# Kernel tuning notes

Measured on AMD Instinct MI355X. Metric: run time of the kernel, lower is better.

## Reference

```python
import jax, jax.numpy as jnp
import numpy as np

D = 1024   # dim_model
H = 16     # num_heads
DH = D // H  # per-head dim for k and v
B, S = 2, 2048
EPS = 1e-5


def layer_norm(x, g, b):
    mu = jnp.mean(x, axis=-1, keepdims=True)
    var = jnp.var(x, axis=-1, keepdims=True)
    return (x - mu) * jax.lax.rsqrt(var + EPS) * g + b


def setup_inputs() -> dict:
    key = jax.random.key(0)
    ks = jax.random.split(key, 8)
    s_d = 1.0 / np.sqrt(D)
    inp = {
        "x": jax.random.normal(ks[0], (B, S, D), dtype=jnp.float32),
        # stacked per-head projections, [H, D, DH] (torch Linear weight.T per head)
        "wq": jax.random.uniform(ks[1], (H, D, DH), jnp.float32, -s_d, s_d),
        "wk": jax.random.uniform(ks[2], (H, D, DH), jnp.float32, -s_d, s_d),
        "wv": jax.random.uniform(ks[3], (H, D, DH), jnp.float32, -s_d, s_d),
        "wo": jax.random.uniform(ks[4], (D, D), jnp.float32, -s_d, s_d),
        "w1": jax.random.uniform(ks[5], (D, D), jnp.float32, -s_d, s_d),  # FFN hidden == dim_model per source
        "w2": jax.random.uniform(ks[6], (D, D), jnp.float32, -s_d, s_d),
        "ln1_g": jnp.ones((D,), jnp.float32), "ln1_b": jnp.zeros((D,), jnp.float32),
        "ln2_g": jnp.ones((D,), jnp.float32), "ln2_b": jnp.zeros((D,), jnp.float32),
        "ln3_g": jnp.ones((D,), jnp.float32), "ln3_b": jnp.zeros((D,), jnp.float32),
    }
    return inp


def reference(x, wq, wk, wv, wo, w1, w2, ln1_g, ln1_b, ln2_g, ln2_b, ln3_g, ln3_b):
    residual = x
    h = layer_norm(x, ln1_g, ln1_b)  # pre_attention_norm
    # batched multi-head attention (equivalent to per-head loop + concat)
    q = jnp.einsum("bsd,hdk->bhsk", h, wq)
    k = jnp.einsum("bsd,hdk->bhsk", h, wk)
    v = jnp.einsum("bsd,hdk->bhsk", h, wv)
    scores = jnp.einsum("bhsk,bhtk->bhst", q, k) / jnp.sqrt(jnp.float32(DH))
    attn = jax.nn.softmax(scores, axis=-1)
    ctx = jnp.einsum("bhst,bhtk->bhsk", attn, v)        # [B,H,S,DH]
    concat = ctx.transpose(0, 2, 1, 3).reshape(x.shape[0], x.shape[1], -1)  # head concat order
    h = concat @ wo
    h = h + residual
    h = layer_norm(h, ln2_g, ln2_b)  # post_attention_norm (dropout is identity, rate=0)
    residual = h
    ffn = jnp.maximum(h @ w1, 0.0) @ w2
    h = ffn + residual
    h = layer_norm(h, ln3_g, ln3_b)  # post_ffn_norm
    return h
```

## Files before the change

### kernel.cpp

```cpp
#include <hip/hip_runtime.h>
#include <stdint.h>

typedef unsigned short u16;
typedef __attribute__((ext_vector_type(8))) short short8;
typedef __attribute__((ext_vector_type(4))) short short4v;
typedef __attribute__((ext_vector_type(4))) float f32x4;

#define DEV static __device__ __forceinline__

constexpr int DMODEL = 1024;
constexpr int SEQ = 2048;

DEV u16 f2b(float f){
  uint32_t u = __float_as_uint(f);
  u += 0x7FFF + ((u >> 16) & 1);
  return (u16)(u >> 16);
}

#define AS1(p) ((const __attribute__((address_space(1))) void*)(p))
#define AS3(p) ((__attribute__((address_space(3))) void*)(p))
#define GLOAD_LDS16(g, l) __builtin_amdgcn_global_load_lds(AS1(g), AS3(l), 16, 0, 0)
#define LDSADDR(p) ((uint32_t)(size_t)((__attribute__((address_space(3))) void*)(p)))

DEV short4v ds_tr16(uint32_t a){
  short4v r;
  asm volatile("ds_read_b64_tr_b16 %0, %1" : "=v"(r) : "v"(a) : "memory");
  return r;
}

DEV void pswap(uint32_t &a, uint32_t &b){
  asm("v_permlane32_swap_b32 %0, %1":"+v"(a),"+v"(b));
  asm("v_permlane16_swap_b32 %0, %1":"+v"(a),"+v"(b));
}

DEV uint32_t cvtpk(float lo, float hi){
  uint32_t r; asm("v_cvt_pk_bf16_f32 %0, %1, %2":"=v"(r):"v"(lo),"v"(hi)); return r;
}

__global__ __launch_bounds__(256) void transpose_generic(
    const float* __restrict__ src, u16* __restrict__ dst, int R, int C){
  __shared__ float tile[64][65];
  int r0 = blockIdx.x*64, c0 = blockIdx.y*64;
  int j = threadIdx.x & 63, i0 = threadIdx.x >> 6;
  for(int i=i0;i<64;i+=4) tile[i][j] = src[(size_t)(r0+i)*C + c0 + j];
  __syncthreads();
  int ii = threadIdx.x & 63, jj0 = threadIdx.x >> 6;
  for(int jj=jj0;jj<64;jj+=4) dst[(size_t)(c0+jj)*R + r0 + ii] = f2b(tile[ii][jj]);
}

__global__ __launch_bounds__(256) void transpose_qkv(
    const float* __restrict__ wq, const float* __restrict__ wk,
    const float* __restrict__ wv, u16* __restrict__ dst){
  int z = blockIdx.z, p = z>>4, h = z&15;
  const float* src = (p==0?wq:(p==1?wk:wv)) + (size_t)h*1024*64;
  float sc = (p==0) ? 0.18033688011112042f : 1.0f;
  __shared__ float tile[64][65];
  int r0 = blockIdx.x*64;
  int j = threadIdx.x & 63, i0 = threadIdx.x >> 6;
  for(int i=i0;i<64;i+=4) tile[i][j] = src[(size_t)(r0+i)*64 + j];
  __syncthreads();
  u16* drow = dst + ((size_t)p*1024 + h*64)*1024;
  int ii = threadIdx.x & 63, jj0 = threadIdx.x >> 6;
  for(int jj=jj0;jj<64;jj+=4) drow[(size_t)jj*1024 + r0 + ii] = f2b(tile[ii][jj]*sc);
}

__global__ __launch_bounds__(256) void ln_kernel(
    const float* __restrict__ in, const float* __restrict__ g, const float* __restrict__ bb,
    u16* __restrict__ outb, float* __restrict__ outf){
  int row = blockIdx.x, tid = threadIdx.x;
  const float4* x4 = (const float4*)(in + (size_t)row*DMODEL);
  float4 v = x4[tid];
  float s  = v.x+v.y+v.z+v.w;
  float ss = v.x*v.x + v.y*v.y + v.z*v.z + v.w*v.w;
  #pragma unroll
  for(int m=1;m<64;m<<=1){ s += __shfl_xor(s,m); ss += __shfl_xor(ss,m); }
  __shared__ float red[8];
  int w = tid>>6;
  if((tid&63)==0){ red[w]=s; red[4+w]=ss; }
  __syncthreads();
  s  = red[0]+red[1]+red[2]+red[3];
  ss = red[4]+red[5]+red[6]+red[7];
  float mu  = s*(1.f/DMODEL);
  float var = ss*(1.f/DMODEL) - mu*mu;
  float rs  = rsqrtf(var + 1e-5f);
  float4 gv = ((const float4*)g)[tid];
  float4 bv = ((const float4*)bb)[tid];
  float y0=(v.x-mu)*rs*gv.x+bv.x, y1=(v.y-mu)*rs*gv.y+bv.y;
  float y2=(v.z-mu)*rs*gv.z+bv.z, y3=(v.w-mu)*rs*gv.w+bv.w;
  if(outb){ ushort4 o = make_ushort4(f2b(y0),f2b(y1),f2b(y2),f2b(y3));
            ((ushort4*)outb)[(size_t)row*(DMODEL/4) + tid] = o; }
  if(outf){ ((float4*)outf)[(size_t)row*(DMODEL/4) + tid] = make_float4(y0,y1,y2,y3); }
}

template<int MODE>
__global__ __launch_bounds__(256) void gemm_bt(
    const u16* __restrict__ A, const u16* __restrict__ BT, int M, int N, int K,
    float* __restrict__ outf, u16* __restrict__ outb, const float* __restrict__ res,
    u16* __restrict__ oq, u16* __restrict__ ok, u16* __restrict__ ov){
  __shared__ u16 lsA[4][2048];
  __shared__ u16 lsB[4][4096];
  int n0 = blockIdx.x*128, m0 = blockIdx.y*64;
  int tid = threadIdx.x, lane = tid&63, w = tid>>6;
  int wr = w>>1, wc = w&1, rq = lane&15, hk = lane>>4;
  int oa = tid*16;
  int ob0 = tid*16, ob1 = 4096 + tid*16;
  const u16* aS  = A  + (size_t)(m0 + (oa>>6))*K  + ((oa&63)>>1);
  const u16* bS0 = BT + (size_t)(n0 + (ob0>>6))*K + ((ob0&63)>>1);
  const u16* bS1 = BT + (size_t)(n0 + (ob1>>6))*K + ((ob1&63)>>1);
  int nk = K>>5;
  f32x4 acc[2][4] = {};
  #pragma unroll
  for(int t=0;t<3;++t){
    GLOAD_LDS16(aS  + t*32, &lsA[t][w*512]);
    GLOAD_LDS16(bS0 + t*32, &lsB[t][w*512]);
    GLOAD_LDS16(bS1 + t*32, &lsB[t][2048 + w*512]);
  }
  for(int kt=0; kt<nk; ++kt){
    if(kt < nk-2)       asm volatile("s_waitcnt vmcnt(6)" ::: "memory");
    else if(kt == nk-2) asm volatile("s_waitcnt vmcnt(3)" ::: "memory");
    else                asm volatile("s_waitcnt vmcnt(0)" ::: "memory");
    __builtin_amdgcn_s_barrier();
    __builtin_amdgcn_sched_barrier(0);
    if(kt+3 < nk){
      int nb = (kt+3)&3;
      GLOAD_LDS16(aS  + (kt+3)*32, &lsA[nb][w*512]);
      GLOAD_LDS16(bS0 + (kt+3)*32, &lsB[nb][w*512]);
      GLOAD_LDS16(bS1 + (kt+3)*32, &lsB[nb][2048 + w*512]);
    }
    const u16* la = &lsA[kt&3][0];
    const u16* lb = &lsB[kt&3][0];
    short8 aF[2], bF[4];
    #pragma unroll
    for(int m=0;m<2;++m) aF[m] = *(const short8*)(la + (wr*32 + m*16 + rq)*32 + hk*8);
    #pragma unroll
    for(int n=0;n<4;++n) bF[n] = *(const short8*)(lb + (wc*64 + n*16 + rq)*32 + hk*8);
    __builtin_amdgcn_s_setprio(1);
    #pragma unroll
    for(int m=0;m<2;++m){
      #pragma unroll
      for(int n=0;n<4;++n)
        acc[m][n] = __builtin_amdgcn_mfma_f32_16x16x32_bf16(aF[m], bF[n], acc[m][n], 0,0,0);
    }
    __builtin_amdgcn_s_setprio(0);
  }
  #pragma unroll
  for(int m=0;m<2;++m){
    #pragma unroll
    for(int n=0;n<4;++n){
      int rb = m0 + wr*32 + m*16 + (hk<<2);
      int c  = n0 + wc*64 + n*16 + rq;
      #pragma unroll
      for(int qq=0;qq<4;++qq){
        int r = rb+qq; float val = acc[m][n][qq];
        if constexpr(MODE==1){
          int proj=c>>10, n1=c&1023, h=n1>>6, d2=n1&63;
          int b=r>>11, si=r&2047;
          u16* dst = proj==0?oq:(proj==1?ok:ov);
          dst[(((size_t)(b*16+h))*SEQ + si)*64 + d2] = f2b(val);
        } else if constexpr(MODE==2){
          outf[(size_t)r*N + c] = val + res[(size_t)r*N + c];
        } else if constexpr(MODE==3){
          outb[(size_t)r*N + c] = f2b(val>0.f?val:0.f);
        } else {
          outb[(size_t)r*N + c] = f2b(val);
        }
      }
    }
  }
}

__global__ __launch_bounds__(256) void attn_kernel(
    const u16* __restrict__ q, const u16* __restrict__ k, const u16* __restrict__ v,
    u16* __restrict__ concat){
  __shared__ u16 lsK[2][4096];
  __shared__ u16 lsV[2][4096];
  int qt = blockIdx.x, bh = blockIdx.y;
  const u16* qp = q + (size_t)bh*SEQ*64;
  const u16* kp = k + (size_t)bh*SEQ*64;
  const u16* vp = v + (size_t)bh*SEQ*64;
  int tid=threadIdx.x, lane=tid&63, w=tid>>6;
  int rq = lane&15, hk = lane>>4;
  const uint32_t sw = (uint32_t)((rq&7)<<4);

  short8 aQ[2];
  {
    const u16* qrow = qp + (size_t)(qt*64 + w*16 + rq)*64 + hk*8;
    aQ[0] = *(const short8*)(qrow);
    aQ[1] = *(const short8*)(qrow + 32);
  }
  short8 bOnes;
  #pragma unroll
  for(int j=0;j<8;++j) bOnes[j] = (short)0x3F80;

  int o0 = tid*16,        kr0 = o0>>7;
  int o1 = 4096 + tid*16, kr1 = o1>>7;
  int koff0 = kr0*64 + ((((o0&127) ^ ((kr0&7)<<4)))>>1);
  int koff1 = kr1*64 + ((((o1&127) ^ ((kr1&7)<<4)))>>1);
  auto vdec = [](int c)->int{
    int t  = ((c>>5)<<2) | ((c&7)>>1);
    int d8 = (((c>>3)&3)<<1) | (c&1);
    return t*64 + d8*8;
  };
  int voff0 = vdec(tid), voff1 = vdec(256+tid);

  f32x4 accO[4] = {};
  f32x4 accL = {};

  GLOAD_LDS16(kp + koff0, &lsK[0][0   + w*512]);
  GLOAD_LDS16(kp + koff1, &lsK[0][2048+ w*512]);
  GLOAD_LDS16(vp + voff0, &lsV[0][0   + w*512]);
  GLOAD_LDS16(vp + voff1, &lsV[0][2048+ w*512]);

  int cur = 0;
  for(int kt=0; kt<SEQ/64; ++kt){
    __syncthreads();
    if(kt+1 < SEQ/64){
      int b = cur^1;
      const u16* ksrc = kp + (kt+1)*4096;
      const u16* vsrc = vp + (kt+1)*4096;
      GLOAD_LDS16(ksrc + koff0, &lsK[b][0   + w*512]);
      GLOAD_LDS16(ksrc + koff1, &lsK[b][2048+ w*512]);
      GLOAD_LDS16(vsrc + voff0, &lsV[b][0   + w*512]);
      GLOAD_LDS16(vsrc + voff1, &lsV[b][2048+ w*512]);
    }
    const char* kb = (const char*)&lsK[cur][0];
    short8 bK[4][2];
    #pragma unroll
    for(int ts=0;ts<4;++ts){
      uint32_t rb = (uint32_t)((ts*16+rq)*128);
      bK[ts][0] = *(const short8*)(kb + rb + (((0u<<6)|(uint32_t)(hk<<4)) ^ sw));
      bK[ts][1] = *(const short8*)(kb + rb + (((1u<<6)|(uint32_t)(hk<<4)) ^ sw));
    }
    f32x4 z[4];
    __builtin_amdgcn_s_setprio(1);
    #pragma unroll
    for(int ts=0;ts<4;++ts){
      f32x4 zz = {};
      zz = __builtin_amdgcn_mfma_f32_16x16x32_bf16(bK[ts][0], aQ[0], zz, 0,0,0);
      zz = __builtin_amdgcn_mfma_f32_16x16x32_bf16(bK[ts][1], aQ[1], zz, 0,0,0);
      z[ts] = zz;
    }
    __builtin_amdgcn_s_setprio(0);
    uint32_t vA = LDSADDR(&lsV[cur][0]) + (uint32_t)(hk*1024 + rq*2);
    short4v vL[2][4][2];
    #pragma unroll
    for(int kh=0;kh<2;++kh){
      #pragma unroll
      for(int ds=0;ds<4;++ds){
        vL[kh][ds][0] = ds_tr16(vA + kh*4096 + ds*128);
        vL[kh][ds][1] = ds_tr16(vA + kh*4096 + ds*128 + 512);
      }
    }
    #pragma unroll
    for(int ts=0;ts<4;++ts){
      #pragma unroll
      for(int r=0;r<4;++r)
        z[ts][r] = __builtin_exp2f(z[ts][r]);
    }
    uint32_t u00=cvtpk(z[0][0],z[0][1]), u01=cvtpk(z[0][2],z[0][3]);
    uint32_t u10=cvtpk(z[1][0],z[1][1]), u11=cvtpk(z[1][2],z[1][3]);
    uint32_t u20=cvtpk(z[2][0],z[2][1]), u21=cvtpk(z[2][2],z[2][3]);
    uint32_t u30=cvtpk(z[3][0],z[3][1]), u31=cvtpk(z[3][2],z[3][3]);
    pswap(u00,u10); pswap(u01,u11);
    pswap(u20,u30); pswap(u21,u31);
    union U8 { uint32_t d[4]; short8 v; } ap0, ap1;
    ap0.d[0]=u00; ap0.d[1]=u01; ap0.d[2]=u10; ap0.d[3]=u11;
    ap1.d[0]=u20; ap1.d[1]=u21; ap1.d[2]=u30; ap1.d[3]=u31;
    asm volatile("s_waitcnt lgkmcnt(0)" ::: "memory");
    __builtin_amdgcn_sched_barrier(0);
    __builtin_amdgcn_s_setprio(1);
    #pragma unroll
    for(int kh=0;kh<2;++kh){
      short8 aP = kh ? ap1.v : ap0.v;
      accL = __builtin_amdgcn_mfma_f32_16x16x32_bf16(aP, bOnes, accL, 0,0,0);
      #pragma unroll
      for(int ds=0;ds<4;++ds){
        short8 bV = __builtin_shufflevector(vL[kh][ds][0], vL[kh][ds][1], 0,1,2,3,4,5,6,7);
        accO[ds] = __builtin_amdgcn_mfma_f32_16x16x32_bf16(aP, bV, accO[ds], 0,0,0);
      }
    }
    __builtin_amdgcn_s_setprio(0);
    cur ^= 1;
  }
  int b = bh>>4, h = bh&15;
  #pragma unroll
  for(int r=0;r<4;++r){
    float inv = 1.f / accL[r];
    int si = qt*64 + w*16 + hk*4 + r;
    #pragma unroll
    for(int ds=0;ds<4;++ds){
      int c = h*64 + ds*16 + rq;
      concat[((size_t)b*SEQ + si)*DMODEL + c] = f2b(accO[ds][r] * inv);
    }
  }
}

extern "C" void kernel_launch(void* const* d_in, const int* in_sizes, int n_in,
                              void* d_out, int out_size, void* d_ws, size_t ws_size,
                              hipStream_t stream){
  (void)in_sizes; (void)n_in; (void)out_size; (void)ws_size;
  const float* x    = (const float*)d_in[0];
  const float* wq   = (const float*)d_in[1];
  const float* wk   = (const float*)d_in[2];
  const float* wv   = (const float*)d_in[3];
  const float* wo   = (const float*)d_in[4];
  const float* w1   = (const float*)d_in[5];
  const float* w2   = (const float*)d_in[6];
  const float* ln1g = (const float*)d_in[7];
  const float* ln1b = (const float*)d_in[8];
  const float* ln2g = (const float*)d_in[9];
  const float* ln2b = (const float*)d_in[10];
  const float* ln3g = (const float*)d_in[11];
  const float* ln3b = (const float*)d_in[12];
  float* out = (float*)d_out;

  char* ws = (char*)d_ws; size_t off = 0;
  auto alloc = [&](size_t b)->char*{ char* p = ws + off; off += (b + 255) & ~(size_t)255; return p; };
  u16*   WqkvT = (u16*)  alloc((size_t)3072*1024*2);
  u16*   WoT   = (u16*)  alloc((size_t)1024*1024*2);
  u16*   W1T   = (u16*)  alloc((size_t)1024*1024*2);
  u16*   W2T   = (u16*)  alloc((size_t)1024*1024*2);
  u16*   h1    = (u16*)  alloc((size_t)4096*1024*2);
  u16*   qb    = (u16*)  alloc((size_t)4194304*2);
  u16*   kb    = (u16*)  alloc((size_t)4194304*2);
  u16*   vb    = (u16*)  alloc((size_t)4194304*2);
  u16*   cc    = (u16*)  alloc((size_t)4096*1024*2);
  float* r1    = (float*)alloc((size_t)4096*1024*4);
  u16*   h2b   = (u16*)  alloc((size_t)4096*1024*2);
  float* h2f   = (float*)alloc((size_t)4096*1024*4);
  u16*   ffn1  = h1;
  float* r2    = r1;

  transpose_qkv<<<dim3(16,1,48),256,0,stream>>>(wq,wk,wv,WqkvT);
  transpose_generic<<<dim3(16,16),256,0,stream>>>(wo,WoT,1024,1024);
  transpose_generic<<<dim3(16,16),256,0,stream>>>(w1,W1T,1024,1024);
  transpose_generic<<<dim3(16,16),256,0,stream>>>(w2,W2T,1024,1024);

  ln_kernel<<<4096,256,0,stream>>>(x, ln1g, ln1b, h1, nullptr);
  gemm_bt<1><<<dim3(24,64),256,0,stream>>>(h1,WqkvT,4096,3072,1024,
      nullptr,nullptr,nullptr, qb,kb,vb);
  attn_kernel<<<dim3(32,32),256,0,stream>>>(qb,kb,vb,cc);
  gemm_bt<2><<<dim3(8,64),256,0,stream>>>(cc,WoT,4096,1024,1024,
      r1,nullptr,x, nullptr,nullptr,nullptr);
  ln_kernel<<<4096,256,0,stream>>>(r1, ln2g, ln2b, h2b, h2f);
  gemm_bt<3><<<dim3(8,64),256,0,stream>>>(h2b,W1T,4096,1024,1024,
      nullptr,ffn1,nullptr, nullptr,nullptr,nullptr);
  gemm_bt<2><<<dim3(8,64),256,0,stream>>>(ffn1,W2T,4096,1024,1024,
      r2,nullptr,h2f, nullptr,nullptr,nullptr);
  ln_kernel<<<4096,256,0,stream>>>(r2, ln3g, ln3b, nullptr, out);
}
```

Measured before the change: 221.1 us.

## Enlarge GEMM and attention tiles, store QKV interleaved, merge weight transposes

GEMM block tile grows from 64x128 to 128x128, doubling per-block A loads and accumulators. The attention kernel now processes 128 query rows per block, two 16-row groups per wave, so each K/V tile loaded into LDS is reused twice as much. The QKV projection writes a plain row-major [4096,3072] buffer that attention reads with strided addressing, removing the scatter epilogue. The four weight-transpose launches are merged into one. Larger tiles raise register pressure and cut the block count, which may hurt occupancy and load balance.

```diff
diff --git a/kernel.cpp b/kernel.cpp
--- a/kernel.cpp
+++ b/kernel.cpp
@@ -37,31 +37,35 @@
   uint32_t r; asm("v_cvt_pk_bf16_f32 %0, %1, %2":"=v"(r):"v"(lo),"v"(hi)); return r;
 }
 
-__global__ __launch_bounds__(256) void transpose_generic(
-    const float* __restrict__ src, u16* __restrict__ dst, int R, int C){
+__global__ __launch_bounds__(256) void transpose_all(
+    const float* __restrict__ wq, const float* __restrict__ wk,
+    const float* __restrict__ wv, const float* __restrict__ wo,
+    const float* __restrict__ w1, const float* __restrict__ w2,
+    u16* __restrict__ WqkvT, u16* __restrict__ WoT,
+    u16* __restrict__ W1T, u16* __restrict__ W2T){
   __shared__ float tile[64][65];
-  int r0 = blockIdx.x*64, c0 = blockIdx.y*64;
+  int bid = blockIdx.x;
   int j = threadIdx.x & 63, i0 = threadIdx.x >> 6;
-  for(int i=i0;i<64;i+=4) tile[i][j] = src[(size_t)(r0+i)*C + c0 + j];
-  __syncthreads();
-  int ii = threadIdx.x & 63, jj0 = threadIdx.x >> 6;
-  for(int jj=jj0;jj<64;jj+=4) dst[(size_t)(c0+jj)*R + r0 + ii] = f2b(tile[ii][jj]);
-}
-
-__global__ __launch_bounds__(256) void transpose_qkv(
-    const float* __restrict__ wq, const float* __restrict__ wk,
-    const float* __restrict__ wv, u16* __restrict__ dst){
-  int z = blockIdx.z, p = z>>4, h = z&15;
-  const float* src = (p==0?wq:(p==1?wk:wv)) + (size_t)h*1024*64;
-  float sc = (p==0) ? 0.18033688011112042f : 1.0f;
-  __shared__ float tile[64][65];
-  int r0 = blockIdx.x*64;
-  int j = threadIdx.x & 63, i0 = threadIdx.x >> 6;
-  for(int i=i0;i<64;i+=4) tile[i][j] = src[(size_t)(r0+i)*64 + j];
-  __syncthreads();
-  u16* drow = dst + ((size_t)p*1024 + h*64)*1024;
-  int ii = threadIdx.x & 63, jj0 = threadIdx.x >> 6;
-  for(int jj=jj0;jj<64;jj+=4) drow[(size_t)jj*1024 + r0 + ii] = f2b(tile[ii][jj]*sc);
+  if(bid < 768){
+    int xb = bid & 15, z = bid >> 4;
+    int p = z >> 4, h = z & 15;
+    const float* src = (p==0?wq:(p==1?wk:wv)) + (size_t)h*1024*64;
+    float sc = (p==0) ? 0.18033688011112042f : 1.0f;
+    int r0 = xb*64;
+    for(int i=i0;i<64;i+=4) tile[i][j] = src[(size_t)(r0+i)*64 + j];
+    __syncthreads();
+    u16* drow = WqkvT + ((size_t)p*1024 + h*64)*1024;
+    for(int jj=i0;jj<64;jj+=4) drow[(size_t)jj*1024 + r0 + j] = f2b(tile[j][jj]*sc);
+  } else {
+    int t = bid - 768;
+    int which = t >> 8; t &= 255;
+    const float* src = which==0?wo:(which==1?w1:w2);
+    u16* dst = which==0?WoT:(which==1?W1T:W2T);
+    int r0 = (t&15)*64, c0 = (t>>4)*64;
+    for(int i=i0;i<64;i+=4) tile[i][j] = src[(size_t)(r0+i)*1024 + c0 + j];
+    __syncthreads();
+    for(int jj=i0;jj<64;jj+=4) dst[(size_t)(c0+jj)*1024 + r0 + j] = f2b(tile[j][jj]);
+  }
 }
 
 __global__ __launch_bounds__(256) void ln_kernel(
@@ -95,48 +99,49 @@
 template<int MODE>
 __global__ __launch_bounds__(256) void gemm_bt(
     const u16* __restrict__ A, const u16* __restrict__ BT, int M, int N, int K,
-    float* __restrict__ outf, u16* __restrict__ outb, const float* __restrict__ res,
-    u16* __restrict__ oq, u16* __restrict__ ok, u16* __restrict__ ov){
-  __shared__ u16 lsA[4][2048];
+    float* __restrict__ outf, u16* __restrict__ outb, const float* __restrict__ res){
+  __shared__ u16 lsA[4][4096];
   __shared__ u16 lsB[4][4096];
-  int n0 = blockIdx.x*128, m0 = blockIdx.y*64;
+  int n0 = blockIdx.x*128, m0 = blockIdx.y*128;
   int tid = threadIdx.x, lane = tid&63, w = tid>>6;
   int wr = w>>1, wc = w&1, rq = lane&15, hk = lane>>4;
-  int oa = tid*16;
-  int ob0 = tid*16, ob1 = 4096 + tid*16;
-  const u16* aS  = A  + (size_t)(m0 + (oa>>6))*K  + ((oa&63)>>1);
-  const u16* bS0 = BT + (size_t)(n0 + (ob0>>6))*K + ((ob0&63)>>1);
-  const u16* bS1 = BT + (size_t)(n0 + (ob1>>6))*K + ((ob1&63)>>1);
+  int o0 = tid*16, o1 = 4096 + tid*16;
+  const u16* aS0 = A  + (size_t)(m0 + (o0>>6))*K + ((o0&63)>>1);
+  const u16* aS1 = A  + (size_t)(m0 + (o1>>6))*K + ((o1&63)>>1);
+  const u16* bS0 = BT + (size_t)(n0 + (o0>>6))*K + ((o0&63)>>1);
+  const u16* bS1 = BT + (size_t)(n0 + (o1>>6))*K + ((o1&63)>>1);
   int nk = K>>5;
-  f32x4 acc[2][4] = {};
+  f32x4 acc[4][4] = {};
   #pragma unroll
   for(int t=0;t<3;++t){
-    GLOAD_LDS16(aS  + t*32, &lsA[t][w*512]);
+    GLOAD_LDS16(aS0 + t*32, &lsA[t][w*512]);
+    GLOAD_LDS16(aS1 + t*32, &lsA[t][2048 + w*512]);
     GLOAD_LDS16(bS0 + t*32, &lsB[t][w*512]);
     GLOAD_LDS16(bS1 + t*32, &lsB[t][2048 + w*512]);
   }
   for(int kt=0; kt<nk; ++kt){
-    if(kt < nk-2)       asm volatile("s_waitcnt vmcnt(6)" ::: "memory");
-    else if(kt == nk-2) asm volatile("s_waitcnt vmcnt(3)" ::: "memory");
+    if(kt < nk-2)       asm volatile("s_waitcnt vmcnt(8)" ::: "memory");
+    else if(kt == nk-2) asm volatile("s_waitcnt vmcnt(4)" ::: "memory");
     else                asm volatile("s_waitcnt vmcnt(0)" ::: "memory");
     __builtin_amdgcn_s_barrier();
     __builtin_amdgcn_sched_barrier(0);
     if(kt+3 < nk){
       int nb = (kt+3)&3;
-      GLOAD_LDS16(aS  + (kt+3)*32, &lsA[nb][w*512]);
+      GLOAD_LDS16(aS0 + (kt+3)*32, &lsA[nb][w*512]);
+      GLOAD_LDS16(aS1 + (kt+3)*32, &lsA[nb][2048 + w*512]);
       GLOAD_LDS16(bS0 + (kt+3)*32, &lsB[nb][w*512]);
       GLOAD_LDS16(bS1 + (kt+3)*32, &lsB[nb][2048 + w*512]);
     }
     const u16* la = &lsA[kt&3][0];
     const u16* lb = &lsB[kt&3][0];
-    short8 aF[2], bF[4];
-    #pragma unroll
-    for(int m=0;m<2;++m) aF[m] = *(const short8*)(la + (wr*32 + m*16 + rq)*32 + hk*8);
+    short8 aF[4], bF[4];
+    #pragma unroll
+    for(int m=0;m<4;++m) aF[m] = *(const short8*)(la + (wr*64 + m*16 + rq)*32 + hk*8);
     #pragma unroll
     for(int n=0;n<4;++n) bF[n] = *(const short8*)(lb + (wc*64 + n*16 + rq)*32 + hk*8);
     __builtin_amdgcn_s_setprio(1);
     #pragma unroll
-    for(int m=0;m<2;++m){
+    for(int m=0;m<4;++m){
       #pragma unroll
       for(int n=0;n<4;++n)
         acc[m][n] = __builtin_amdgcn_mfma_f32_16x16x32_bf16(aF[m], bF[n], acc[m][n], 0,0,0);
@@ -144,20 +149,15 @@
     __builtin_amdgcn_s_setprio(0);
   }
   #pragma unroll
-  for(int m=0;m<2;++m){
+  for(int m=0;m<4;++m){
     #pragma unroll
     for(int n=0;n<4;++n){
-      int rb = m0 + wr*32 + m*16 + (hk<<2);
+      int rb = m0 + wr*64 + m*16 + (hk<<2);
       int c  = n0 + wc*64 + n*16 + rq;
       #pragma unroll
       for(int qq=0;qq<4;++qq){
         int r = rb+qq; float val = acc[m][n][qq];
-        if constexpr(MODE==1){
-          int proj=c>>10, n1=c&1023, h=n1>>6, d2=n1&63;
-          int b=r>>11, si=r&2047;
-          u16* dst = proj==0?oq:(proj==1?ok:ov);
-          dst[(((size_t)(b*16+h))*SEQ + si)*64 + d2] = f2b(val);
-        } else if constexpr(MODE==2){
+        if constexpr(MODE==2){
           outf[(size_t)r*N + c] = val + res[(size_t)r*N + c];
         } else if constexpr(MODE==3){
           outb[(size_t)r*N + c] = f2b(val>0.f?val:0.f);
@@ -170,23 +170,24 @@
 }
 
 __global__ __launch_bounds__(256) void attn_kernel(
-    const u16* __restrict__ q, const u16* __restrict__ k, const u16* __restrict__ v,
-    u16* __restrict__ concat){
+    const u16* __restrict__ qkv, u16* __restrict__ concat){
   __shared__ u16 lsK[2][4096];
   __shared__ u16 lsV[2][4096];
   int qt = blockIdx.x, bh = blockIdx.y;
-  const u16* qp = q + (size_t)bh*SEQ*64;
-  const u16* kp = k + (size_t)bh*SEQ*64;
-  const u16* vp = v + (size_t)bh*SEQ*64;
+  int b = bh>>4, h = bh&15;
+  const u16* qp = qkv + (size_t)b*2048*3072 + h*64;
+  const u16* kp = qp + 1024;
+  const u16* vp = qp + 2048;
   int tid=threadIdx.x, lane=tid&63, w=tid>>6;
   int rq = lane&15, hk = lane>>4;
   const uint32_t sw = (uint32_t)((rq&7)<<4);
 
-  short8 aQ[2];
-  {
-    const u16* qrow = qp + (size_t)(qt*64 + w*16 + rq)*64 + hk*8;
-    aQ[0] = *(const short8*)(qrow);
-    aQ[1] = *(const short8*)(qrow + 32);
+  short8 aQ[2][2];
+  #pragma unroll
+  for(int qg=0;qg<2;++qg){
+    const u16* qrow = qp + (size_t)(qt*128 + w*32 + qg*16 + rq)*3072 + hk*8;
+    aQ[qg][0] = *(const short8*)(qrow);
+    aQ[qg][1] = *(const short8*)(qrow + 32);
   }
   short8 bOnes;
   #pragma unroll
@@ -194,53 +195,69 @@
 
   int o0 = tid*16,        kr0 = o0>>7;
   int o1 = 4096 + tid*16, kr1 = o1>>7;
-  int koff0 = kr0*64 + ((((o0&127) ^ ((kr0&7)<<4)))>>1);
-  int koff1 = kr1*64 + ((((o1&127) ^ ((kr1&7)<<4)))>>1);
-  auto vdec = [](int c)->int{
-    int t  = ((c>>5)<<2) | ((c&7)>>1);
-    int d8 = (((c>>3)&3)<<1) | (c&1);
-    return t*64 + d8*8;
-  };
-  int voff0 = vdec(tid), voff1 = vdec(256+tid);
-
-  f32x4 accO[4] = {};
-  f32x4 accL = {};
-
-  GLOAD_LDS16(kp + koff0, &lsK[0][0   + w*512]);
-  GLOAD_LDS16(kp + koff1, &lsK[0][2048+ w*512]);
-  GLOAD_LDS16(vp + voff0, &lsV[0][0   + w*512]);
-  GLOAD_LDS16(vp + voff1, &lsV[0][2048+ w*512]);
+  const u16* kS0 = kp + (size_t)kr0*3072 + ((((o0&127) ^ ((kr0&7)<<4)))>>1);
+  const u16* kS1 = kp + (size_t)kr1*3072 + ((((o1&127) ^ ((kr1&7)<<4)))>>1);
+  int c0v = tid,      vt0 = ((c0v>>5)<<2)|((c0v&7)>>1), vd0 = (((c0v>>3)&3)<<1)|(c0v&1);
+  int c1v = 256+tid,  vt1 = ((c1v>>5)<<2)|((c1v&7)>>1), vd1 = (((c1v>>3)&3)<<1)|(c1v&1);
+  const u16* vS0 = vp + (size_t)vt0*3072 + vd0*8;
+  const u16* vS1 = vp + (size_t)vt1*3072 + vd1*8;
+  const size_t TS = (size_t)64*3072;
+
+  f32x4 accO[2][4] = {};
+  f32x4 accL[2] = {};
+
+  GLOAD_LDS16(kS0, &lsK[0][w*512]);
+  GLOAD_LDS16(kS1, &lsK[0][2048+w*512]);
+  GLOAD_LDS16(vS0, &lsV[0][w*512]);
+  GLOAD_LDS16(vS1, &lsV[0][2048+w*512]);
 
   int cur = 0;
   for(int kt=0; kt<SEQ/64; ++kt){
     __syncthreads();
     if(kt+1 < SEQ/64){
-      int b = cur^1;
-      const u16* ksrc = kp + (kt+1)*4096;
-      const u16* vsrc = vp + (kt+1)*4096;
-      GLOAD_LDS16(ksrc + koff0, &lsK[b][0   + w*512]);
-      GLOAD_LDS16(ksrc + koff1, &lsK[b][2048+ w*512]);
-      GLOAD_LDS16(vsrc + voff0, &lsV[b][0   + w*512]);
-      GLOAD_LDS16(vsrc + voff1, &lsV[b][2048+ w*512]);
+      int nb = cur^1;
+      GLOAD_LDS16(kS0 + (kt+1)*TS, &lsK[nb][w*512]);
+      GLOAD_LDS16(kS1 + (kt+1)*TS, &lsK[nb][2048+w*512]);
+      GLOAD_LDS16(vS0 + (kt+1)*TS, &lsV[nb][w*512]);
+      GLOAD_LDS16(vS1 + (kt+1)*TS, &lsV[nb][2048+w*512]);
     }
     const char* kb = (const char*)&lsK[cur][0];
-    short8 bK[4][2];
-    #pragma unroll
-    for(int ts=0;ts<4;++ts){
-      uint32_t rb = (uint32_t)((ts*16+rq)*128);
-      bK[ts][0] = *(const short8*)(kb + rb + (((0u<<6)|(uint32_t)(hk<<4)) ^ sw));
-      bK[ts][1] = *(const short8*)(kb + rb + (((1u<<6)|(uint32_t)(hk<<4)) ^ sw));
-    }
-    f32x4 z[4];
-    __builtin_amdgcn_s_setprio(1);
-    #pragma unroll
-    for(int ts=0;ts<4;++ts){
-      f32x4 zz = {};
-      zz = __builtin_amdgcn_mfma_f32_16x16x32_bf16(bK[ts][0], aQ[0], zz, 0,0,0);
-      zz = __builtin_amdgcn_mfma_f32_16x16x32_bf16(bK[ts][1], aQ[1], zz, 0,0,0);
-      z[ts] = zz;
-    }
-    __builtin_amdgcn_s_setprio(0);
+    uint32_t apk[2][2][4];
+    #pragma unroll
+    for(int tp=0; tp<2; ++tp){
+      short8 bK[2][2];
+      #pragma unroll
+      for(int t2=0;t2<2;++t2){
+        uint32_t rb = (uint32_t)(((tp*2+t2)*16+rq)*128);
+        bK[t2][0] = *(const short8*)(kb + rb + (((uint32_t)(hk<<4)) ^ sw));
+        bK[t2][1] = *(const short8*)(kb + rb + ((64u|(uint32_t)(hk<<4)) ^ sw));
+      }
+      f32x4 z[2][2];
+      __builtin_amdgcn_s_setprio(1);
+      #pragma unroll
+      for(int qg=0;qg<2;++qg){
+        #pragma unroll
+        for(int t2=0;t2<2;++t2){
+          f32x4 zz = {};
+          zz = __builtin_amdgcn_mfma_f32_16x16x32_bf16(bK[t2][0], aQ[qg][0], zz, 0,0,0);
+          zz = __builtin_amdgcn_mfma_f32_16x16x32_bf16(bK[t2][1], aQ[qg][1], zz, 0,0,0);
+          z[qg][t2] = zz;
+        }
+      }
+      __builtin_amdgcn_s_setprio(0);
+      #pragma unroll
+      for(int qg=0;qg<2;++qg){
+        #pragma unroll
+        for(int t2=0;t2<2;++t2){
+          #pragma unroll
+          for(int r=0;r<4;++r) z[qg][t2][r] = __builtin_exp2f(z[qg][t2][r]);
+        }
+        uint32_t a0=cvtpk(z[qg][0][0],z[qg][0][1]), a1=cvtpk(z[qg][0][2],z[qg][0][3]);
+        uint32_t b0=cvtpk(z[qg][1][0],z[qg][1][1]), b1=cvtpk(z[qg][1][2],z[qg][1][3]);
+        pswap(a0,b0); pswap(a1,b1);
+        apk[tp][qg][0]=a0; apk[tp][qg][1]=a1; apk[tp][qg][2]=b0; apk[tp][qg][3]=b1;
+      }
+    }
     uint32_t vA = LDSADDR(&lsV[cur][0]) + (uint32_t)(hk*1024 + rq*2);
     short4v vL[2][4][2];
     #pragma unroll
@@ -251,46 +268,38 @@
         vL[kh][ds][1] = ds_tr16(vA + kh*4096 + ds*128 + 512);
       }
     }
-    #pragma unroll
-    for(int ts=0;ts<4;++ts){
-      #pragma unroll
-      for(int r=0;r<4;++r)
-        z[ts][r] = __builtin_exp2f(z[ts][r]);
-    }
-    uint32_t u00=cvtpk(z[0][0],z[0][1]), u01=cvtpk(z[0][2],z[0][3]);
-    uint32_t u10=cvtpk(z[1][0],z[1][1]), u11=cvtpk(z[1][2],z[1][3]);
-    uint32_t u20=cvtpk(z[2][0],z[2][1]), u21=cvtpk(z[2][2],z[2][3]);
-    uint32_t u30=cvtpk(z[3][0],z[3][1]), u31=cvtpk(z[3][2],z[3][3]);
-    pswap(u00,u10); pswap(u01,u11);
-    pswap(u20,u30); pswap(u21,u31);
-    union U8 { uint32_t d[4]; short8 v; } ap0, ap1;
-    ap0.d[0]=u00; ap0.d[1]=u01; ap0.d[2]=u10; ap0.d[3]=u11;
-    ap1.d[0]=u20; ap1.d[1]=u21; ap1.d[2]=u30; ap1.d[3]=u31;
     asm volatile("s_waitcnt lgkmcnt(0)" ::: "memory");
     __builtin_amdgcn_sched_barrier(0);
     __builtin_amdgcn_s_setprio(1);
     #pragma unroll
     for(int kh=0;kh<2;++kh){
-      short8 aP = kh ? ap1.v : ap0.v;
-      accL = __builtin_amdgcn_mfma_f32_16x16x32_bf16(aP, bOnes, accL, 0,0,0);
-      #pragma unroll
-      for(int ds=0;ds<4;++ds){
-        short8 bV = __builtin_shufflevector(vL[kh][ds][0], vL[kh][ds][1], 0,1,2,3,4,5,6,7);
-        accO[ds] = __builtin_amdgcn_mfma_f32_16x16x32_bf16(aP, bV, accO[ds], 0,0,0);
+      #pragma unroll
+      for(int qg=0;qg<2;++qg){
+        union U8 { uint32_t d[4]; short8 v; } ap;
+        ap.d[0]=apk[kh][qg][0]; ap.d[1]=apk[kh][qg][1];
+        ap.d[2]=apk[kh][qg][2]; ap.d[3]=apk[kh][qg][3];
+        accL[qg] = __builtin_amdgcn_mfma_f32_16x16x32_bf16(ap.v, bOnes, accL[qg], 0,0,0);
+        #pragma unroll
+        for(int ds=0;ds<4;++ds){
+          short8 bV = __builtin_shufflevector(vL[kh][ds][0], vL[kh][ds][1], 0,1,2,3,4,5,6,7);
+          accO[qg][ds] = __builtin_amdgcn_mfma_f32_16x16x32_bf16(ap.v, bV, accO[qg][ds], 0,0,0);
+        }
       }
     }
     __builtin_amdgcn_s_setprio(0);
     cur ^= 1;
   }
-  int b = bh>>4, h = bh&15;
-  #pragma unroll
-  for(int r=0;r<4;++r){
-    float inv = 1.f / accL[r];
-    int si = qt*64 + w*16 + hk*4 + r;
-    #pragma unroll
-    for(int ds=0;ds<4;++ds){
-      int c = h*64 + ds*16 + rq;
-      concat[((size_t)b*SEQ + si)*DMODEL + c] = f2b(accO[ds][r] * inv);
+  #pragma unroll
+  for(int qg=0;qg<2;++qg){
+    #pragma unroll
+    for(int r=0;r<4;++r){
+      float inv = 1.f / accL[qg][r];
+      int si = qt*128 + w*32 + qg*16 + hk*4 + r;
+      #pragma unroll
+      for(int ds=0;ds<4;++ds){
+        int c = h*64 + ds*16 + rq;
+        concat[((size_t)b*SEQ + si)*DMODEL + c] = f2b(accO[qg][ds][r] * inv);
+      }
     }
   }
 }
@@ -321,9 +330,7 @@
   u16*   W1T   = (u16*)  alloc((size_t)1024*1024*2);
   u16*   W2T   = (u16*)  alloc((size_t)1024*1024*2);
   u16*   h1    = (u16*)  alloc((size_t)4096*1024*2);
-  u16*   qb    = (u16*)  alloc((size_t)4194304*2);
-  u16*   kb    = (u16*)  alloc((size_t)4194304*2);
-  u16*   vb    = (u16*)  alloc((size_t)4194304*2);
+  u16*   qkv   = (u16*)  alloc((size_t)4096*3072*2);
   u16*   cc    = (u16*)  alloc((size_t)4096*1024*2);
   float* r1    = (float*)alloc((size_t)4096*1024*4);
   u16*   h2b   = (u16*)  alloc((size_t)4096*1024*2);
@@ -331,21 +338,18 @@
   u16*   ffn1  = h1;
   float* r2    = r1;
 
-  transpose_qkv<<<dim3(16,1,48),256,0,stream>>>(wq,wk,wv,WqkvT);
-  transpose_generic<<<dim3(16,16),256,0,stream>>>(wo,WoT,1024,1024);
-  transpose_generic<<<dim3(16,16),256,0,stream>>>(w1,W1T,1024,1024);
-  transpose_generic<<<dim3(16,16),256,0,stream>>>(w2,W2T,1024,1024);
+  transpose_all<<<1536,256,0,stream>>>(wq,wk,wv,wo,w1,w2, WqkvT,WoT,W1T,W2T);
 
   ln_kernel<<<4096,256,0,stream>>>(x, ln1g, ln1b, h1, nullptr);
-  gemm_bt<1><<<dim3(24,64),256,0,stream>>>(h1,WqkvT,4096,3072,1024,
-      nullptr,nullptr,nullptr, qb,kb,vb);
-  attn_kernel<<<dim3(32,32),256,0,stream>>>(qb,kb,vb,cc);
-  gemm_bt<2><<<dim3(8,64),256,0,stream>>>(cc,WoT,4096,1024,1024,
-      r1,nullptr,x, nullptr,nullptr,nullptr);
+  gemm_bt<0><<<dim3(24,32),256,0,stream>>>(h1,WqkvT,4096,3072,1024,
+      nullptr,qkv,nullptr);
+  attn_kernel<<<dim3(16,32),256,0,stream>>>(qkv,cc);
+  gemm_bt<2><<<dim3(8,32),256,0,stream>>>(cc,WoT,4096,1024,1024,
+      r1,nullptr,x);
   ln_kernel<<<4096,256,0,stream>>>(r1, ln2g, ln2b, h2b, h2f);
-  gemm_bt<3><<<dim3(8,64),256,0,stream>>>(h2b,W1T,4096,1024,1024,
-      nullptr,ffn1,nullptr, nullptr,nullptr,nullptr);
-  gemm_bt<2><<<dim3(8,64),256,0,stream>>>(ffn1,W2T,4096,1024,1024,
-      r2,nullptr,h2f, nullptr,nullptr,nullptr);
+  gemm_bt<3><<<dim3(8,32),256,0,stream>>>(h2b,W1T,4096,1024,1024,
+      nullptr,ffn1,nullptr);
+  gemm_bt<2><<<dim3(8,32),256,0,stream>>>(ffn1,W2T,4096,1024,1024,
+      r2,nullptr,h2f);
   ln_kernel<<<4096,256,0,stream>>>(r2, ln3g, ln3b, nullptr, out);
 }
```

Result: slower. 227.2 us (+2.8%).
